# Performance work log

Measured on AMD Instinct MI355X. Metric: run time of the kernel, lower is better.

Reference implementation:

```python
import jax, jax.numpy as jnp
import numpy as np

N_NODES = 50000
N_EDGES = 800000
D_IN = 64
D_HID = 128  # out_channels * expansion(2)
EPS_MSG = 1e-7
EPS_SOFTMAX = 1e-16
EPS_BN = 1e-5
N_LAYERS = 4


def mish(x):
    return x * jnp.tanh(jax.nn.softplus(x))


def setup_inputs() -> dict:
    key = jax.random.key(0)
    ks = jax.random.split(key, 8)
    x = jax.random.normal(ks[0], (N_NODES, D_IN), dtype=jnp.float32)
    edge_index = jax.random.randint(ks[1], (2, N_EDGES), 0, N_NODES, dtype=jnp.int64)
    # Per-layer GENConv MLP params: Linear(64->128), BN(128), ReLU, Linear(128->64)
    s1 = 1.0 / np.sqrt(D_IN)
    s2 = 1.0 / np.sqrt(D_HID)
    W1 = jax.random.uniform(ks[2], (N_LAYERS, D_IN, D_HID), jnp.float32, -s1, s1)
    b1 = jax.random.uniform(ks[3], (N_LAYERS, D_HID), jnp.float32, -s1, s1)
    gamma = jnp.ones((N_LAYERS, D_HID), jnp.float32)
    beta = jnp.zeros((N_LAYERS, D_HID), jnp.float32)
    W2 = jax.random.uniform(ks[4], (N_LAYERS, D_HID, D_IN), jnp.float32, -s2, s2)
    b2 = jax.random.uniform(ks[5], (N_LAYERS, D_IN), jnp.float32, -s2, s2)
    return {"x": x, "edge_index": edge_index, "W1": W1, "b1": b1,
            "gamma": gamma, "beta": beta, "W2": W2, "b2": b2}


def gen_conv(x, src, dst, W1, b1, gamma, beta, W2, b2):
    n = x.shape[0]
    # message: relu(x_j) + eps  -> [E, D]
    msg = jax.nn.relu(x[src]) + EPS_MSG
    # softmax aggregation (t=1) per destination node, per feature channel
    m = jax.ops.segment_max(msg, dst, num_segments=n)
    e = jnp.exp(msg - m[dst])
    denom = jax.ops.segment_sum(e, dst, num_segments=n)[dst] + EPS_SOFTMAX
    alpha = e / denom
    agg = jax.ops.segment_sum(msg * alpha, dst, num_segments=n)
    # residual with destination features, then 2-layer MLP w/ BatchNorm (train mode)
    h = agg + x
    h = h @ W1 + b1
    mu = jnp.mean(h, axis=0)
    var = jnp.var(h, axis=0)  # biased, as torch BN uses for normalization
    h = (h - mu) * jax.lax.rsqrt(var + EPS_BN) * gamma + beta
    h = jax.nn.relu(h)
    return h @ W2 + b2


def reference(x, edge_index, W1, b1, gamma, beta, W2, b2):
    src, dst = edge_index[0], edge_index[1]
    h = x
    for i in range(N_LAYERS):
        h = gen_conv(h, src, dst, W1[i], b1[i], gamma[i], beta[i], W2[i], b2[i])
        if i < N_LAYERS - 1:
            h = mish(h)
    return h
```

## Files before the change

### kernel.cpp

```cpp
#include <hip/hip_runtime.h>
#include <math.h>

#define N_NODES 50000
#define N_EDGES 800000
#define D_IN 64
#define D_HID 128
#define SCAN_B 256
#define N_SB ((N_NODES + SCAN_B - 1) / SCAN_B)
#define NPB 256
#define NB ((N_NODES + NPB - 1) / NPB)
#define P1_BLOCKS 256
#define EPB (N_EDGES / P1_BLOCKS)

typedef unsigned short u16;
typedef unsigned int u32;
typedef __attribute__((ext_vector_type(8))) short short8;
typedef __attribute__((ext_vector_type(4))) float f32x4;

union U4S8 { uint4 u; short8 s; };

__device__ __forceinline__ float bf2f(u16 u) {
    u32 x = ((u32)u) << 16;
    float f; __builtin_memcpy(&f, &x, 4); return f;
}
__device__ __forceinline__ u16 f2bf(float f) {
    u32 x; __builtin_memcpy(&x, &f, 4);
    x += 0x7fffu + ((x >> 16) & 1u);
    return (u16)(x >> 16);
}
__device__ __forceinline__ u32 pk2(float a, float b) {
    return (u32)f2bf(a) | ((u32)f2bf(b) << 16);
}


__global__ void count_kernel(const int* __restrict__ dst, int* __restrict__ deg, int E) {
    int i = blockIdx.x * blockDim.x + threadIdx.x;
    if (i < E) atomicAdd(&deg[dst[i]], 1);
}

__global__ __launch_bounds__(SCAN_B) void scan_reduce_kernel(const int* __restrict__ deg,
                                                             int* __restrict__ bsum) {
    __shared__ int s[SCAN_B];
    int i = blockIdx.x * SCAN_B + threadIdx.x;
    int v = (i < N_NODES) ? deg[i] : 0;
    s[threadIdx.x] = v;
    __syncthreads();
    #pragma unroll
    for (int o = SCAN_B / 2; o > 0; o >>= 1) {
        if (threadIdx.x < o) s[threadIdx.x] += s[threadIdx.x + o];
        __syncthreads();
    }
    if (threadIdx.x == 0) bsum[blockIdx.x] = s[0];
}

__global__ __launch_bounds__(SCAN_B) void scan_sums_kernel(const int* __restrict__ bsum,
                                                           int* __restrict__ boff) {
    __shared__ int s[SCAN_B];
    int t = threadIdx.x;
    int v = (t < N_SB) ? bsum[t] : 0;
    s[t] = v;
    __syncthreads();
    #pragma unroll
    for (int o = 1; o < SCAN_B; o <<= 1) {
        int u = (t >= o) ? s[t - o] : 0;
        __syncthreads();
        s[t] += u;
        __syncthreads();
    }
    if (t < N_SB) boff[t] = s[t] - v;
}

__global__ __launch_bounds__(SCAN_B) void scan_write_kernel(const int* __restrict__ deg,
                                                            const int* __restrict__ boff,
                                                            int* __restrict__ off) {
    __shared__ int s[SCAN_B];
    int t = threadIdx.x;
    int i = blockIdx.x * SCAN_B + t;
    int v = (i < N_NODES) ? deg[i] : 0;
    s[t] = v;
    __syncthreads();
    #pragma unroll
    for (int o = 1; o < SCAN_B; o <<= 1) {
        int u = (t >= o) ? s[t - o] : 0;
        __syncthreads();
        s[t] += u;
        __syncthreads();
    }
    int incl = s[t] + boff[blockIdx.x];
    if (i < N_NODES) off[i] = incl - v;
    if (i == N_NODES - 1) off[N_NODES] = incl;
}

__global__ void bin_init_kernel(const int* __restrict__ off, int* __restrict__ gcur) {
    int b = threadIdx.x;
    if (b < NB) gcur[b] = off[min(b * NPB, N_NODES)];
}

__global__ __launch_bounds__(256) void bin_pass1_kernel(const int* __restrict__ src,
                                                        const int* __restrict__ dst,
                                                        int* __restrict__ gcur,
                                                        int2* __restrict__ ebuf) {
    __shared__ int hist[NB];
    __shared__ int base[NB];
    const int tid = threadIdx.x;
    const int e0 = blockIdx.x * EPB, e1 = e0 + EPB;
    for (int b = tid; b < NB; b += 256) hist[b] = 0;
    __syncthreads();
    for (int i = e0 + tid; i < e1; i += 256)
        atomicAdd(&hist[dst[i] >> 8], 1);
    __syncthreads();
    for (int b = tid; b < NB; b += 256) {
        base[b] = atomicAdd(&gcur[b], hist[b]);
        hist[b] = 0;
    }
    __syncthreads();
    for (int i = e0 + tid; i < e1; i += 256) {
        int d = dst[i];
        int b = d >> 8;
        int slot = base[b] + atomicAdd(&hist[b], 1);
        ebuf[slot] = make_int2(src[i], d);
    }
}

__global__ __launch_bounds__(256) void bin_pass2_kernel(const int* __restrict__ off,
                                                        const int2* __restrict__ ebuf,
                                                        int* __restrict__ esrc) {
    __shared__ int soff[NPB];
    __shared__ int cur[NPB];
    const int b = blockIdx.x;
    const int tid = threadIdx.x;
    const int n0 = b * NPB;
    soff[tid] = off[min(n0 + tid, N_NODES)];
    cur[tid] = 0;
    __syncthreads();
    const int e0 = soff[0];
    const int e1 = off[min(n0 + NPB, N_NODES)];
    for (int i = e0 + tid; i < e1; i += 256) {
        int2 p = ebuf[i];
        int dl = p.y - n0;
        int slot = soff[dl] + atomicAdd(&cur[dl], 1);
        esrc[slot] = p.x;
    }
}

__global__ __launch_bounds__(256) void xcvt_kernel(const float* __restrict__ x,
                                                   u16* __restrict__ xb) {
    int i = blockIdx.x * 256 + threadIdx.x;
    if (i < N_NODES * D_IN / 4) {
        float4 v = ((const float4*)x)[i];
        u32 lo = pk2(v.x, v.y), hi = pk2(v.z, v.w);
        ((uint2*)xb)[i] = make_uint2(lo, hi);
    }
}

__global__ __launch_bounds__(256) void wprep_kernel(const float* __restrict__ W1,
                                                    const float* __restrict__ W2,
                                                    u16* __restrict__ w1f,
                                                    u16* __restrict__ w2f) {
    const int b = blockIdx.x;
    const int L = b >> 1;
    if ((b & 1) == 0) {
        const float* W = W1 + (size_t)L * 64 * 128;
        u16* outp = w1f + (size_t)L * 8192;
        for (int idx = threadIdx.x; idx < 1024; idx += 256) {
            int ln = idx & 63, th = idx >> 6;
            int half = th & 1, t = th >> 1;
            int k0 = half * 32 + (ln >> 4) * 8;
            int n = t * 16 + (ln & 15);
            uint4 o;
            o.x = pk2(W[(k0 + 0) * 128 + n], W[(k0 + 1) * 128 + n]);
            o.y = pk2(W[(k0 + 2) * 128 + n], W[(k0 + 3) * 128 + n]);
            o.z = pk2(W[(k0 + 4) * 128 + n], W[(k0 + 5) * 128 + n]);
            o.w = pk2(W[(k0 + 6) * 128 + n], W[(k0 + 7) * 128 + n]);
            *(uint4*)&outp[(size_t)idx * 8] = o;
        }
    } else {
        const float* W = W2 + (size_t)L * 128 * 64;
        u16* outp = w2f + (size_t)L * 8192;
        for (int idx = threadIdx.x; idx < 1024; idx += 256) {
            int ln = idx & 63, th = idx >> 6;
            int ks = th & 3, t = th >> 2;
            int k0 = ks * 32 + (ln >> 4) * 8;
            int n = t * 16 + (ln & 15);
            uint4 o;
            o.x = pk2(W[(k0 + 0) * 64 + n], W[(k0 + 1) * 64 + n]);
            o.y = pk2(W[(k0 + 2) * 64 + n], W[(k0 + 3) * 64 + n]);
            o.z = pk2(W[(k0 + 4) * 64 + n], W[(k0 + 5) * 64 + n]);
            o.w = pk2(W[(k0 + 6) * 64 + n], W[(k0 + 7) * 64 + n]);
            *(uint4*)&outp[(size_t)idx * 8] = o;
        }
    }
}

__global__ __launch_bounds__(256) void agg_kernel(const u16* __restrict__ x,
                                                  const int* __restrict__ off,
                                                  const int* __restrict__ esrc,
                                                  u16* __restrict__ h) {
    const int node = blockIdx.x * 4 + (threadIdx.x >> 6);
    const int ln = threadIdx.x & 63;
    const int e = ln >> 3;
    const int cb = (ln & 7) * 8;
    if (node >= N_NODES) return;
    const int jb = off[node], je = off[node + 1];
    float s[8], t[8];
    #pragma unroll
    for (int k = 0; k < 8; k++) { s[k] = 0.f; t[k] = 0.f; }
    int j = jb;
    for (; j + 16 <= je; j += 16) {
        int i0 = esrc[j + e];
        int i1 = esrc[j + 8 + e];
        U4S8 r0, r1;
        r0.u = *(const uint4*)&x[(size_t)i0 * D_IN + cb];
        r1.u = *(const uint4*)&x[(size_t)i1 * D_IN + cb];
        #pragma unroll
        for (int k = 0; k < 8; k++) {
            float m = fmaxf(bf2f((u16)r0.s[k]), 0.f) + 1e-7f;
            float p = __expf(m);
            s[k] += p; t[k] = fmaf(m, p, t[k]);
        }
        #pragma unroll
        for (int k = 0; k < 8; k++) {
            float m = fmaxf(bf2f((u16)r1.s[k]), 0.f) + 1e-7f;
            float p = __expf(m);
            s[k] += p; t[k] = fmaf(m, p, t[k]);
        }
    }
    int rem = je - j;
    if (rem > 0) {
        bool act = e < rem;
        int idx = esrc[j + (act ? e : rem - 1)];
        U4S8 r;
        r.u = *(const uint4*)&x[(size_t)idx * D_IN + cb];
        if (act) {
            #pragma unroll
            for (int k = 0; k < 8; k++) {
                float m = fmaxf(bf2f((u16)r.s[k]), 0.f) + 1e-7f;
                float p = __expf(m);
                s[k] += p; t[k] = fmaf(m, p, t[k]);
            }
        }
        if (rem > 8) {
            bool act2 = (e + 8) < rem;
            int idx2 = esrc[j + 8 + (act2 ? e : rem - 9)];
            U4S8 r2;
            r2.u = *(const uint4*)&x[(size_t)idx2 * D_IN + cb];
            if (act2) {
                #pragma unroll
                for (int k = 0; k < 8; k++) {
                    float m = fmaxf(bf2f((u16)r2.s[k]), 0.f) + 1e-7f;
                    float p = __expf(m);
                    s[k] += p; t[k] = fmaf(m, p, t[k]);
                }
            }
        }
    }
    #pragma unroll
    for (int k = 0; k < 8; k++) {
        s[k] += __shfl_xor(s[k], 8);
        s[k] += __shfl_xor(s[k], 16);
        s[k] += __shfl_xor(s[k], 32);
        t[k] += __shfl_xor(t[k], 8);
        t[k] += __shfl_xor(t[k], 16);
        t[k] += __shfl_xor(t[k], 32);
    }
    if (e == 0) {
        U4S8 xr;
        xr.u = *(const uint4*)&x[(size_t)node * D_IN + cb];
        u32 w[4];
        #pragma unroll
        for (int k2 = 0; k2 < 4; k2++) {
            float v0 = t[2 * k2]     / (s[2 * k2]     + 1e-16f) + bf2f((u16)xr.s[2 * k2]);
            float v1 = t[2 * k2 + 1] / (s[2 * k2 + 1] + 1e-16f) + bf2f((u16)xr.s[2 * k2 + 1]);
            w[k2] = pk2(v0, v1);
        }
        *(uint4*)&h[(size_t)node * D_IN + cb] = make_uint4(w[0], w[1], w[2], w[3]);
    }
}

#define SC1 136
__global__ __launch_bounds__(256) void gemm1_kernel(const u16* __restrict__ A,
                                                    const u16* __restrict__ Wf,
                                                    const float* __restrict__ bias,
                                                    u16* __restrict__ Bout,
                                                    float* __restrict__ S,
                                                    float* __restrict__ Q) {
    __shared__ u16 sC[64 * SC1];
    const int tid = threadIdx.x;
    const int wave = tid >> 6, ln = tid & 63;
    const int lm = ln & 15, quad = ln >> 4;
    const int row0g = blockIdx.x * 64;
    const int row0 = row0g + wave * 16;
    const int rA = min(row0 + lm, N_NODES - 1);

    U4S8 a0, a1;
    a0.u = *(const uint4*)&A[(size_t)rA * 64 + quad * 8];
    a1.u = *(const uint4*)&A[(size_t)rA * 64 + 32 + quad * 8];

    f32x4 acc[8];
    #pragma unroll
    for (int t = 0; t < 8; t++) {
        float b = bias[t * 16 + lm];
        acc[t] = (f32x4){b, b, b, b};
    }
    #pragma unroll
    for (int t = 0; t < 8; t++) {
        U4S8 b0, b1;
        b0.u = *(const uint4*)&Wf[(size_t)((t * 2 + 0) * 64 + ln) * 8];
        b1.u = *(const uint4*)&Wf[(size_t)((t * 2 + 1) * 64 + ln) * 8];
        acc[t] = __builtin_amdgcn_mfma_f32_16x16x32_bf16(a0.s, b0.s, acc[t], 0, 0, 0);
        acc[t] = __builtin_amdgcn_mfma_f32_16x16x32_bf16(a1.s, b1.s, acc[t], 0, 0, 0);
    }
    const int lr0 = wave * 16 + quad * 4;
    #pragma unroll
    for (int t = 0; t < 8; t++) {
        #pragma unroll
        for (int rg = 0; rg < 4; rg++)
            sC[(lr0 + rg) * SC1 + t * 16 + lm] = f2bf(acc[t][rg]);
    }
    __syncthreads();
    const int c8 = (tid & 15) * 8;
    #pragma unroll
    for (int i = 0; i < 4; i++) {
        int lr = (tid >> 4) + i * 16;
        int r = row0g + lr;
        if (r < N_NODES)
            *(uint4*)&Bout[(size_t)r * 128 + c8] = *(const uint4*)&sC[lr * SC1 + c8];
    }
    const int rlim = min(64, N_NODES - row0g);
    if (tid < 128) {
        float s = 0.f;
        #pragma unroll 8
        for (int r = 0; r < rlim; r++) s += bf2f(sC[r * SC1 + tid]);
        atomicAdd(&S[tid], s);
    } else {
        int c = tid - 128;
        float q = 0.f;
        #pragma unroll 8
        for (int r = 0; r < rlim; r++) { float v = bf2f(sC[r * SC1 + c]); q += v * v; }
        atomicAdd(&Q[c], q);
    }
}

__device__ __forceinline__ float mish_f(float v) {
    if (v > 30.f) return v;
    float u = __expf(v);
    float t = (u + 1.f) * (u + 1.f);
    return v * (t - 1.f) / (t + 1.f);
}

#define SC2B 72
#define SC2F 68
__global__ __launch_bounds__(256) void gemm2_kernel(const u16* __restrict__ H,
                                                    const float* __restrict__ S,
                                                    const float* __restrict__ Q,
                                                    const float* __restrict__ gamma,
                                                    const float* __restrict__ beta,
                                                    const u16* __restrict__ Wf,
                                                    const float* __restrict__ bias,
                                                    float* __restrict__ outf,
                                                    u16* __restrict__ outb,
                                                    int dobf16) {
    __shared__ float sss[256];
    __shared__ __align__(16) char sCraw[64 * SC2F * 4];
    u16* sCb = (u16*)sCraw;
    float* sCf = (float*)sCraw;
    const int tid = threadIdx.x;
    if (tid < 128) {
        float mean = S[tid] * (1.f / N_NODES);
        float var = fmaxf(Q[tid] * (1.f / N_NODES) - mean * mean, 0.f);
        float sc = gamma[tid] * rsqrtf(var + 1e-5f);
        sss[tid] = sc;
        sss[128 + tid] = beta[tid] - mean * sc;
    }
    __syncthreads();
    const int wave = tid >> 6, ln = tid & 63;
    const int lm = ln & 15, quad = ln >> 4;
    const int row0g = blockIdx.x * 64;
    const int row0 = row0g + wave * 16;
    const int rA = min(row0 + lm, N_NODES - 1);

    f32x4 acc[4];
    #pragma unroll
    for (int t = 0; t < 4; t++) {
        float b = bias[t * 16 + lm];
        acc[t] = (f32x4){b, b, b, b};
    }
    #pragma unroll
    for (int ks = 0; ks < 4; ks++) {
        const int k0 = ks * 32 + quad * 8;
        U4S8 h8;
        h8.u = *(const uint4*)&H[(size_t)rA * 128 + k0];
        U4S8 a;
        #pragma unroll
        for (int j2 = 0; j2 < 4; j2++) {
            int k = k0 + 2 * j2;
            float v0 = fmaxf(fmaf(bf2f((u16)h8.s[2 * j2]),     sss[k],     sss[128 + k]),     0.f);
            float v1 = fmaxf(fmaf(bf2f((u16)h8.s[2 * j2 + 1]), sss[k + 1], sss[128 + k + 1]), 0.f);
            ((u32*)&a.u)[j2] = pk2(v0, v1);
        }
        #pragma unroll
        for (int t = 0; t < 4; t++) {
            U4S8 b;
            b.u = *(const uint4*)&Wf[(size_t)((t * 4 + ks) * 64 + ln) * 8];
            acc[t] = __builtin_amdgcn_mfma_f32_16x16x32_bf16(a.s, b.s, acc[t], 0, 0, 0);
        }
    }
    const int lr0 = wave * 16 + quad * 4;
    if (dobf16) {
        #pragma unroll
        for (int t = 0; t < 4; t++) {
            #pragma unroll
            for (int rg = 0; rg < 4; rg++)
                sCb[(lr0 + rg) * SC2B + t * 16 + lm] = f2bf(mish_f(acc[t][rg]));
        }
        __syncthreads();
        const int c8 = (tid & 7) * 8;
        #pragma unroll
        for (int i = 0; i < 2; i++) {
            int lr = (tid >> 3) + i * 32;
            int r = row0g + lr;
            if (r < N_NODES)
                *(uint4*)&outb[(size_t)r * 64 + c8] = *(const uint4*)&sCb[lr * SC2B + c8];
        }
    } else {
        #pragma unroll
        for (int t = 0; t < 4; t++) {
            #pragma unroll
            for (int rg = 0; rg < 4; rg++)
                sCf[(lr0 + rg) * SC2F + t * 16 + lm] = acc[t][rg];
        }
        __syncthreads();
        const int c8 = (tid & 7) * 8;
        #pragma unroll
        for (int i = 0; i < 2; i++) {
            int lr = (tid >> 3) + i * 32;
            int r = row0g + lr;
            if (r < N_NODES) {
                *(float4*)&outf[(size_t)r * 64 + c8]     = *(const float4*)&sCf[lr * SC2F + c8];
                *(float4*)&outf[(size_t)r * 64 + c8 + 4] = *(const float4*)&sCf[lr * SC2F + c8 + 4];
            }
        }
    }
}


extern "C" void kernel_launch(void* const* d_in, const int* in_sizes, int n_in,
                              void* d_out, int out_size, void* d_ws, size_t ws_size,
                              hipStream_t stream) {
    const float* x     = (const float*)d_in[0];
    const int*   ei    = (const int*)d_in[1];
    const float* W1    = (const float*)d_in[2];
    const float* b1    = (const float*)d_in[3];
    const float* gamma = (const float*)d_in[4];
    const float* beta  = (const float*)d_in[5];
    const float* W2    = (const float*)d_in[6];
    const float* b2    = (const float*)d_in[7];
    float* out = (float*)d_out;

    const int* src = ei;
    const int* dst = ei + N_EDGES;

    char* base = (char*)d_ws;
    size_t o = 0;
    auto take = [&](size_t bytes) -> char* {
        char* p = base + o;
        o = (o + bytes + 255) & ~(size_t)255;
        return p;
    };
    int* deg     = (int*)take((size_t)N_NODES * 4);
    int* off     = (int*)take((size_t)(N_NODES + 1) * 4);
    int* esrc    = (int*)take((size_t)N_EDGES * 4);
    int2* ebuf   = (int2*)take((size_t)N_EDGES * 8);
    int* bsum    = (int*)take((size_t)N_SB * 4);
    int* boff    = (int*)take((size_t)N_SB * 4);
    int* gcur    = (int*)take((size_t)NB * 4);
    float* bn    = (float*)take(1024 * 4);
    u16* w1f     = (u16*)take((size_t)4 * 8192 * 2);
    u16* w2f     = (u16*)take((size_t)4 * 8192 * 2);
    u16* xbuf    = (u16*)take((size_t)N_NODES * D_IN * 2);
    u16* hbuf    = (u16*)take((size_t)N_NODES * D_IN * 2);
    u16* h1buf   = (u16*)take((size_t)N_NODES * D_HID * 2);

    hipMemsetAsync(deg, 0, (size_t)N_NODES * 4, stream);
    hipMemsetAsync(bn, 0, 1024 * 4, stream);
    count_kernel<<<(N_EDGES + 255) / 256, 256, 0, stream>>>(dst, deg, N_EDGES);
    scan_reduce_kernel<<<N_SB, SCAN_B, 0, stream>>>(deg, bsum);
    scan_sums_kernel<<<1, SCAN_B, 0, stream>>>(bsum, boff);
    scan_write_kernel<<<N_SB, SCAN_B, 0, stream>>>(deg, boff, off);
    bin_init_kernel<<<1, 256, 0, stream>>>(off, gcur);
    bin_pass1_kernel<<<P1_BLOCKS, 256, 0, stream>>>(src, dst, gcur, ebuf);
    bin_pass2_kernel<<<NB, 256, 0, stream>>>(off, ebuf, esrc);
    xcvt_kernel<<<(N_NODES * D_IN / 4 + 255) / 256, 256, 0, stream>>>(x, xbuf);
    wprep_kernel<<<8, 256, 0, stream>>>(W1, W2, w1f, w2f);

    const int NBLK = (N_NODES + 63) / 64;
    const int ABLK = (N_NODES + 3) / 4;
    for (int L = 0; L < 4; L++) {
        float* Sb = bn + L * 256;
        float* Qb = Sb + 128;
        agg_kernel<<<ABLK, 256, 0, stream>>>(xbuf, off, esrc, hbuf);
        gemm1_kernel<<<NBLK, 256, 0, stream>>>(
            hbuf, w1f + (size_t)L * 8192, b1 + (size_t)L * D_HID, h1buf,
            Sb, Qb);
        gemm2_kernel<<<NBLK, 256, 0, stream>>>(
            h1buf, Sb, Qb, gamma + (size_t)L * D_HID, beta + (size_t)L * D_HID,
            w2f + (size_t)L * 8192, b2 + (size_t)L * D_IN,
            out, xbuf, (L < 3) ? 1 : 0);
    }
}
```

Measured before the change: 438.3 us.

## Split node features into two channel halves and aggregate each half separately

Node features are stored as two 32-channel bf16 arrays, and the aggregation runs twice, once per half, so each gather pass has a smaller working set that fits better in cache. Each aggregation kernel now covers 16 edges per iteration with 4 lanes per row, and uses nontemporal loads and stores for edge indices and outputs. Separately, gemm1 computes the BatchNorm sum and sum-of-squares from fp32 MFMA accumulators through shuffles instead of rescanning bf16 values in shared memory. The cost is twice the edge-index reads and an extra kernel launch per layer.

```diff
diff --git a/kernel.cpp b/kernel.cpp
--- a/kernel.cpp
+++ b/kernel.cpp
@@ -16,6 +16,7 @@
 typedef unsigned int u32;
 typedef __attribute__((ext_vector_type(8))) short short8;
 typedef __attribute__((ext_vector_type(4))) float f32x4;
+typedef __attribute__((ext_vector_type(4))) u32 u32x4;
 
 union U4S8 { uint4 u; short8 s; };
 
@@ -144,12 +145,19 @@
 }
 
 __global__ __launch_bounds__(256) void xcvt_kernel(const float* __restrict__ x,
-                                                   u16* __restrict__ xb) {
+                                                   u16* __restrict__ xlo,
+                                                   u16* __restrict__ xhi) {
     int i = blockIdx.x * 256 + threadIdx.x;
     if (i < N_NODES * D_IN / 4) {
         float4 v = ((const float4*)x)[i];
+        int node = i >> 4;
+        int c4 = (i & 15) * 4;
         u32 lo = pk2(v.x, v.y), hi = pk2(v.z, v.w);
-        ((uint2*)xb)[i] = make_uint2(lo, hi);
+        uint2 o = make_uint2(lo, hi);
+        if (c4 < 32)
+            *(uint2*)&xlo[(size_t)node * 32 + c4] = o;
+        else
+            *(uint2*)&xhi[(size_t)node * 32 + (c4 - 32)] = o;
     }
 }
 
@@ -192,45 +200,39 @@
     }
 }
 
-__global__ __launch_bounds__(256) void agg_kernel(const u16* __restrict__ x,
-                                                  const int* __restrict__ off,
-                                                  const int* __restrict__ esrc,
-                                                  u16* __restrict__ h) {
+__global__ __launch_bounds__(256) void agg32_kernel(const u16* __restrict__ xh,
+                                                    const int* __restrict__ off,
+                                                    const int* __restrict__ esrc,
+                                                    u16* __restrict__ h,
+                                                    int chbase) {
     const int node = blockIdx.x * 4 + (threadIdx.x >> 6);
     const int ln = threadIdx.x & 63;
-    const int e = ln >> 3;
-    const int cb = (ln & 7) * 8;
-    if (node >= N_NODES) return;
+    const int e = ln >> 2;
+    const int cb = (ln & 3) * 8;
     const int jb = off[node], je = off[node + 1];
+    U4S8 xr;
+    xr.u = *(const uint4*)&xh[(size_t)node * 32 + cb];
     float s[8], t[8];
     #pragma unroll
     for (int k = 0; k < 8; k++) { s[k] = 0.f; t[k] = 0.f; }
     int j = jb;
     for (; j + 16 <= je; j += 16) {
-        int i0 = esrc[j + e];
-        int i1 = esrc[j + 8 + e];
-        U4S8 r0, r1;
-        r0.u = *(const uint4*)&x[(size_t)i0 * D_IN + cb];
-        r1.u = *(const uint4*)&x[(size_t)i1 * D_IN + cb];
+        int i0 = __builtin_nontemporal_load(&esrc[j + e]);
+        U4S8 r0;
+        r0.u = *(const uint4*)&xh[(size_t)i0 * 32 + cb];
         #pragma unroll
         for (int k = 0; k < 8; k++) {
             float m = fmaxf(bf2f((u16)r0.s[k]), 0.f) + 1e-7f;
             float p = __expf(m);
             s[k] += p; t[k] = fmaf(m, p, t[k]);
         }
-        #pragma unroll
-        for (int k = 0; k < 8; k++) {
-            float m = fmaxf(bf2f((u16)r1.s[k]), 0.f) + 1e-7f;
-            float p = __expf(m);
-            s[k] += p; t[k] = fmaf(m, p, t[k]);
-        }
     }
     int rem = je - j;
     if (rem > 0) {
         bool act = e < rem;
-        int idx = esrc[j + (act ? e : rem - 1)];
+        int idx = __builtin_nontemporal_load(&esrc[j + (act ? e : 0)]);
         U4S8 r;
-        r.u = *(const uint4*)&x[(size_t)idx * D_IN + cb];
+        r.u = *(const uint4*)&xh[(size_t)idx * 32 + cb];
         if (act) {
             #pragma unroll
             for (int k = 0; k < 8; k++) {
@@ -239,41 +241,23 @@
                 s[k] += p; t[k] = fmaf(m, p, t[k]);
             }
         }
-        if (rem > 8) {
-            bool act2 = (e + 8) < rem;
-            int idx2 = esrc[j + 8 + (act2 ? e : rem - 9)];
-            U4S8 r2;
-            r2.u = *(const uint4*)&x[(size_t)idx2 * D_IN + cb];
-            if (act2) {
-                #pragma unroll
-                for (int k = 0; k < 8; k++) {
-                    float m = fmaxf(bf2f((u16)r2.s[k]), 0.f) + 1e-7f;
-                    float p = __expf(m);
-                    s[k] += p; t[k] = fmaf(m, p, t[k]);
-                }
-            }
-        }
     }
     #pragma unroll
     for (int k = 0; k < 8; k++) {
-        s[k] += __shfl_xor(s[k], 8);
-        s[k] += __shfl_xor(s[k], 16);
-        s[k] += __shfl_xor(s[k], 32);
-        t[k] += __shfl_xor(t[k], 8);
-        t[k] += __shfl_xor(t[k], 16);
-        t[k] += __shfl_xor(t[k], 32);
+        s[k] += __shfl_xor(s[k], 4);  s[k] += __shfl_xor(s[k], 8);
+        s[k] += __shfl_xor(s[k], 16); s[k] += __shfl_xor(s[k], 32);
+        t[k] += __shfl_xor(t[k], 4);  t[k] += __shfl_xor(t[k], 8);
+        t[k] += __shfl_xor(t[k], 16); t[k] += __shfl_xor(t[k], 32);
     }
     if (e == 0) {
-        U4S8 xr;
-        xr.u = *(const uint4*)&x[(size_t)node * D_IN + cb];
-        u32 w[4];
+        u32x4 w;
         #pragma unroll
         for (int k2 = 0; k2 < 4; k2++) {
             float v0 = t[2 * k2]     / (s[2 * k2]     + 1e-16f) + bf2f((u16)xr.s[2 * k2]);
             float v1 = t[2 * k2 + 1] / (s[2 * k2 + 1] + 1e-16f) + bf2f((u16)xr.s[2 * k2 + 1]);
             w[k2] = pk2(v0, v1);
         }
-        *(uint4*)&h[(size_t)node * D_IN + cb] = make_uint4(w[0], w[1], w[2], w[3]);
+        __builtin_nontemporal_store(w, (u32x4*)&h[(size_t)node * 64 + chbase + cb]);
     }
 }
 
@@ -285,6 +269,7 @@
                                                     float* __restrict__ S,
                                                     float* __restrict__ Q) {
     __shared__ u16 sC[64 * SC1];
+    __shared__ float sRed[2][4][128];
     const int tid = threadIdx.x;
     const int wave = tid >> 6, ln = tid & 63;
     const int lm = ln & 15, quad = ln >> 4;
@@ -310,6 +295,24 @@
         acc[t] = __builtin_amdgcn_mfma_f32_16x16x32_bf16(a0.s, b0.s, acc[t], 0, 0, 0);
         acc[t] = __builtin_amdgcn_mfma_f32_16x16x32_bf16(a1.s, b1.s, acc[t], 0, 0, 0);
     }
+    const int rbase = row0 + quad * 4;
+    #pragma unroll
+    for (int t = 0; t < 8; t++) {
+        float ss = 0.f, qq = 0.f;
+        #pragma unroll
+        for (int rg = 0; rg < 4; rg++) {
+            if (rbase + rg < N_NODES) {
+                float v = acc[t][rg];
+                ss += v; qq = fmaf(v, v, qq);
+            }
+        }
+        ss += __shfl_xor(ss, 16); ss += __shfl_xor(ss, 32);
+        qq += __shfl_xor(qq, 16); qq += __shfl_xor(qq, 32);
+        if (quad == 0) {
+            sRed[0][wave][t * 16 + lm] = ss;
+            sRed[1][wave][t * 16 + lm] = qq;
+        }
+    }
     const int lr0 = wave * 16 + quad * 4;
     #pragma unroll
     for (int t = 0; t < 8; t++) {
@@ -326,18 +329,13 @@
         if (r < N_NODES)
             *(uint4*)&Bout[(size_t)r * 128 + c8] = *(const uint4*)&sC[lr * SC1 + c8];
     }
-    const int rlim = min(64, N_NODES - row0g);
     if (tid < 128) {
-        float s = 0.f;
-        #pragma unroll 8
-        for (int r = 0; r < rlim; r++) s += bf2f(sC[r * SC1 + tid]);
-        atomicAdd(&S[tid], s);
+        float v = sRed[0][0][tid] + sRed[0][1][tid] + sRed[0][2][tid] + sRed[0][3][tid];
+        atomicAdd(&S[tid], v);
     } else {
         int c = tid - 128;
-        float q = 0.f;
-        #pragma unroll 8
-        for (int r = 0; r < rlim; r++) { float v = bf2f(sC[r * SC1 + c]); q += v * v; }
-        atomicAdd(&Q[c], q);
+        float v = sRed[1][0][c] + sRed[1][1][c] + sRed[1][2][c] + sRed[1][3][c];
+        atomicAdd(&Q[c], v);
     }
 }
 
@@ -358,7 +356,8 @@
                                                     const u16* __restrict__ Wf,
                                                     const float* __restrict__ bias,
                                                     float* __restrict__ outf,
-                                                    u16* __restrict__ outb,
+                                                    u16* __restrict__ xlo,
+                                                    u16* __restrict__ xhi,
                                                     int dobf16) {
     __shared__ float sss[256];
     __shared__ __align__(16) char sCraw[64 * SC2F * 4];
@@ -419,8 +418,13 @@
         for (int i = 0; i < 2; i++) {
             int lr = (tid >> 3) + i * 32;
             int r = row0g + lr;
-            if (r < N_NODES)
-                *(uint4*)&outb[(size_t)r * 64 + c8] = *(const uint4*)&sCb[lr * SC2B + c8];
+            if (r < N_NODES) {
+                uint4 val = *(const uint4*)&sCb[lr * SC2B + c8];
+                if (c8 < 32)
+                    *(uint4*)&xlo[(size_t)r * 32 + c8] = val;
+                else
+                    *(uint4*)&xhi[(size_t)r * 32 + (c8 - 32)] = val;
+            }
         }
     } else {
         #pragma unroll
@@ -477,7 +481,8 @@
     float* bn    = (float*)take(1024 * 4);
     u16* w1f     = (u16*)take((size_t)4 * 8192 * 2);
     u16* w2f     = (u16*)take((size_t)4 * 8192 * 2);
-    u16* xbuf    = (u16*)take((size_t)N_NODES * D_IN * 2);
+    u16* xlo     = (u16*)take((size_t)N_NODES * 32 * 2);
+    u16* xhi     = (u16*)take((size_t)N_NODES * 32 * 2);
     u16* hbuf    = (u16*)take((size_t)N_NODES * D_IN * 2);
     u16* h1buf   = (u16*)take((size_t)N_NODES * D_HID * 2);
 
@@ -490,7 +495,7 @@
     bin_init_kernel<<<1, 256, 0, stream>>>(off, gcur);
     bin_pass1_kernel<<<P1_BLOCKS, 256, 0, stream>>>(src, dst, gcur, ebuf);
     bin_pass2_kernel<<<NB, 256, 0, stream>>>(off, ebuf, esrc);
-    xcvt_kernel<<<(N_NODES * D_IN / 4 + 255) / 256, 256, 0, stream>>>(x, xbuf);
+    xcvt_kernel<<<(N_NODES * D_IN / 4 + 255) / 256, 256, 0, stream>>>(x, xlo, xhi);
     wprep_kernel<<<8, 256, 0, stream>>>(W1, W2, w1f, w2f);
 
     const int NBLK = (N_NODES + 63) / 64;
@@ -498,13 +503,14 @@
     for (int L = 0; L < 4; L++) {
         float* Sb = bn + L * 256;
         float* Qb = Sb + 128;
-        agg_kernel<<<ABLK, 256, 0, stream>>>(xbuf, off, esrc, hbuf);
+        agg32_kernel<<<ABLK, 256, 0, stream>>>(xlo, off, esrc, hbuf, 0);
+        agg32_kernel<<<ABLK, 256, 0, stream>>>(xhi, off, esrc, hbuf, 32);
         gemm1_kernel<<<NBLK, 256, 0, stream>>>(
             hbuf, w1f + (size_t)L * 8192, b1 + (size_t)L * D_HID, h1buf,
             Sb, Qb);
         gemm2_kernel<<<NBLK, 256, 0, stream>>>(
             h1buf, Sb, Qb, gamma + (size_t)L * D_HID, beta + (size_t)L * D_HID,
             w2f + (size_t)L * 8192, b2 + (size_t)L * D_IN,
-            out, xbuf, (L < 3) ? 1 : 0);
-    }
-}
+            out, xlo, xhi, (L < 3) ? 1 : 0);
+    }
+}
```

Result: slower. 598.6 us (+36.6%).

## Precompute ReLU'd bf16 features and compute BN stats from accumulators

Applied to the files above, without the earlier changes.

Producer kernels now write a second bf16 buffer holding relu(x), so the gather loop in aggregation skips the max and epsilon add per element. The constant epsilon is added after normalisation, which is exact because the softmax weights sum to about one. The exp is also taken without the epsilon, which changes rounding slightly. Gemm1 now reduces BN sum and sum-of-squares from fp32 MFMA accumulators with wave shuffles and a small shared buffer, replacing the serial 64-row loop over bf16 shared memory. The cost is an extra 6.4 MB buffer and an extra store per layer.

```diff
diff --git a/kernel.cpp b/kernel.cpp
--- a/kernel.cpp
+++ b/kernel.cpp
@@ -31,6 +31,12 @@
 __device__ __forceinline__ u32 pk2(float a, float b) {
     return (u32)f2bf(a) | ((u32)f2bf(b) << 16);
 }
+__device__ __forceinline__ u32 relu2(u32 w) {
+    u32 b = (w >> 15) & 0x00010001u;
+    u32 m01 = b ^ 0x00010001u;
+    u32 M = (m01 << 16) - m01;
+    return w & M;
+}
 
 
 __global__ void count_kernel(const int* __restrict__ dst, int* __restrict__ deg, int E) {
@@ -144,12 +150,14 @@
 }
 
 __global__ __launch_bounds__(256) void xcvt_kernel(const float* __restrict__ x,
-                                                   u16* __restrict__ xb) {
+                                                   u16* __restrict__ xb,
+                                                   u16* __restrict__ rb) {
     int i = blockIdx.x * 256 + threadIdx.x;
     if (i < N_NODES * D_IN / 4) {
         float4 v = ((const float4*)x)[i];
         u32 lo = pk2(v.x, v.y), hi = pk2(v.z, v.w);
         ((uint2*)xb)[i] = make_uint2(lo, hi);
+        ((uint2*)rb)[i] = make_uint2(relu2(lo), relu2(hi));
     }
 }
 
@@ -192,7 +200,8 @@
     }
 }
 
-__global__ __launch_bounds__(256) void agg_kernel(const u16* __restrict__ x,
+__global__ __launch_bounds__(256) void agg_kernel(const u16* __restrict__ xb,
+                                                  const u16* __restrict__ rb,
                                                   const int* __restrict__ off,
                                                   const int* __restrict__ esrc,
                                                   u16* __restrict__ h) {
@@ -202,6 +211,8 @@
     const int cb = (ln & 7) * 8;
     if (node >= N_NODES) return;
     const int jb = off[node], je = off[node + 1];
+    U4S8 xr;
+    xr.u = *(const uint4*)&xb[(size_t)node * D_IN + cb];
     float s[8], t[8];
     #pragma unroll
     for (int k = 0; k < 8; k++) { s[k] = 0.f; t[k] = 0.f; }
@@ -210,17 +221,17 @@
         int i0 = esrc[j + e];
         int i1 = esrc[j + 8 + e];
         U4S8 r0, r1;
-        r0.u = *(const uint4*)&x[(size_t)i0 * D_IN + cb];
-        r1.u = *(const uint4*)&x[(size_t)i1 * D_IN + cb];
+        r0.u = *(const uint4*)&rb[(size_t)i0 * D_IN + cb];
+        r1.u = *(const uint4*)&rb[(size_t)i1 * D_IN + cb];
         #pragma unroll
         for (int k = 0; k < 8; k++) {
-            float m = fmaxf(bf2f((u16)r0.s[k]), 0.f) + 1e-7f;
+            float m = bf2f((u16)r0.s[k]);
             float p = __expf(m);
             s[k] += p; t[k] = fmaf(m, p, t[k]);
         }
         #pragma unroll
         for (int k = 0; k < 8; k++) {
-            float m = fmaxf(bf2f((u16)r1.s[k]), 0.f) + 1e-7f;
+            float m = bf2f((u16)r1.s[k]);
             float p = __expf(m);
             s[k] += p; t[k] = fmaf(m, p, t[k]);
         }
@@ -230,11 +241,11 @@
         bool act = e < rem;
         int idx = esrc[j + (act ? e : rem - 1)];
         U4S8 r;
-        r.u = *(const uint4*)&x[(size_t)idx * D_IN + cb];
+        r.u = *(const uint4*)&rb[(size_t)idx * D_IN + cb];
         if (act) {
             #pragma unroll
             for (int k = 0; k < 8; k++) {
-                float m = fmaxf(bf2f((u16)r.s[k]), 0.f) + 1e-7f;
+                float m = bf2f((u16)r.s[k]);
                 float p = __expf(m);
                 s[k] += p; t[k] = fmaf(m, p, t[k]);
             }
@@ -243,11 +254,11 @@
             bool act2 = (e + 8) < rem;
             int idx2 = esrc[j + 8 + (act2 ? e : rem - 9)];
             U4S8 r2;
-            r2.u = *(const uint4*)&x[(size_t)idx2 * D_IN + cb];
+            r2.u = *(const uint4*)&rb[(size_t)idx2 * D_IN + cb];
             if (act2) {
                 #pragma unroll
                 for (int k = 0; k < 8; k++) {
-                    float m = fmaxf(bf2f((u16)r2.s[k]), 0.f) + 1e-7f;
+                    float m = bf2f((u16)r2.s[k]);
                     float p = __expf(m);
                     s[k] += p; t[k] = fmaf(m, p, t[k]);
                 }
@@ -264,13 +275,11 @@
         t[k] += __shfl_xor(t[k], 32);
     }
     if (e == 0) {
-        U4S8 xr;
-        xr.u = *(const uint4*)&x[(size_t)node * D_IN + cb];
         u32 w[4];
         #pragma unroll
         for (int k2 = 0; k2 < 4; k2++) {
-            float v0 = t[2 * k2]     / (s[2 * k2]     + 1e-16f) + bf2f((u16)xr.s[2 * k2]);
-            float v1 = t[2 * k2 + 1] / (s[2 * k2 + 1] + 1e-16f) + bf2f((u16)xr.s[2 * k2 + 1]);
+            float v0 = t[2 * k2]     / (s[2 * k2]     + 1e-16f) + 1e-7f + bf2f((u16)xr.s[2 * k2]);
+            float v1 = t[2 * k2 + 1] / (s[2 * k2 + 1] + 1e-16f) + 1e-7f + bf2f((u16)xr.s[2 * k2 + 1]);
             w[k2] = pk2(v0, v1);
         }
         *(uint4*)&h[(size_t)node * D_IN + cb] = make_uint4(w[0], w[1], w[2], w[3]);
@@ -285,6 +294,7 @@
                                                     float* __restrict__ S,
                                                     float* __restrict__ Q) {
     __shared__ u16 sC[64 * SC1];
+    __shared__ float sRed[2][4][128];
     const int tid = threadIdx.x;
     const int wave = tid >> 6, ln = tid & 63;
     const int lm = ln & 15, quad = ln >> 4;
@@ -310,6 +320,24 @@
         acc[t] = __builtin_amdgcn_mfma_f32_16x16x32_bf16(a0.s, b0.s, acc[t], 0, 0, 0);
         acc[t] = __builtin_amdgcn_mfma_f32_16x16x32_bf16(a1.s, b1.s, acc[t], 0, 0, 0);
     }
+    const int rbase = row0 + quad * 4;
+    #pragma unroll
+    for (int t = 0; t < 8; t++) {
+        float ss = 0.f, qq = 0.f;
+        #pragma unroll
+        for (int rg = 0; rg < 4; rg++) {
+            if (rbase + rg < N_NODES) {
+                float v = acc[t][rg];
+                ss += v; qq = fmaf(v, v, qq);
+            }
+        }
+        ss += __shfl_xor(ss, 16); ss += __shfl_xor(ss, 32);
+        qq += __shfl_xor(qq, 16); qq += __shfl_xor(qq, 32);
+        if (quad == 0) {
+            sRed[0][wave][t * 16 + lm] = ss;
+            sRed[1][wave][t * 16 + lm] = qq;
+        }
+    }
     const int lr0 = wave * 16 + quad * 4;
     #pragma unroll
     for (int t = 0; t < 8; t++) {
@@ -326,18 +354,13 @@
         if (r < N_NODES)
             *(uint4*)&Bout[(size_t)r * 128 + c8] = *(const uint4*)&sC[lr * SC1 + c8];
     }
-    const int rlim = min(64, N_NODES - row0g);
     if (tid < 128) {
-        float s = 0.f;
-        #pragma unroll 8
-        for (int r = 0; r < rlim; r++) s += bf2f(sC[r * SC1 + tid]);
-        atomicAdd(&S[tid], s);
+        float v = sRed[0][0][tid] + sRed[0][1][tid] + sRed[0][2][tid] + sRed[0][3][tid];
+        atomicAdd(&S[tid], v);
     } else {
         int c = tid - 128;
-        float q = 0.f;
-        #pragma unroll 8
-        for (int r = 0; r < rlim; r++) { float v = bf2f(sC[r * SC1 + c]); q += v * v; }
-        atomicAdd(&Q[c], q);
+        float v = sRed[1][0][c] + sRed[1][1][c] + sRed[1][2][c] + sRed[1][3][c];
+        atomicAdd(&Q[c], v);
     }
 }
 
@@ -358,7 +381,8 @@
                                                     const u16* __restrict__ Wf,
                                                     const float* __restrict__ bias,
                                                     float* __restrict__ outf,
-                                                    u16* __restrict__ outb,
+                                                    u16* __restrict__ xb,
+                                                    u16* __restrict__ rb,
                                                     int dobf16) {
     __shared__ float sss[256];
     __shared__ __align__(16) char sCraw[64 * SC2F * 4];
@@ -419,8 +443,14 @@
         for (int i = 0; i < 2; i++) {
             int lr = (tid >> 3) + i * 32;
             int r = row0g + lr;
-            if (r < N_NODES)
-                *(uint4*)&outb[(size_t)r * 64 + c8] = *(const uint4*)&sCb[lr * SC2B + c8];
+            if (r < N_NODES) {
+                uint4 val = *(const uint4*)&sCb[lr * SC2B + c8];
+                *(uint4*)&xb[(size_t)r * 64 + c8] = val;
+                uint4 rv;
+                rv.x = relu2(val.x); rv.y = relu2(val.y);
+                rv.z = relu2(val.z); rv.w = relu2(val.w);
+                *(uint4*)&rb[(size_t)r * 64 + c8] = rv;
+            }
         }
     } else {
         #pragma unroll
@@ -478,6 +508,7 @@
     u16* w1f     = (u16*)take((size_t)4 * 8192 * 2);
     u16* w2f     = (u16*)take((size_t)4 * 8192 * 2);
     u16* xbuf    = (u16*)take((size_t)N_NODES * D_IN * 2);
+    u16* rbuf    = (u16*)take((size_t)N_NODES * D_IN * 2);
     u16* hbuf    = (u16*)take((size_t)N_NODES * D_IN * 2);
     u16* h1buf   = (u16*)take((size_t)N_NODES * D_HID * 2);
 
@@ -490,7 +521,7 @@
     bin_init_kernel<<<1, 256, 0, stream>>>(off, gcur);
     bin_pass1_kernel<<<P1_BLOCKS, 256, 0, stream>>>(src, dst, gcur, ebuf);
     bin_pass2_kernel<<<NB, 256, 0, stream>>>(off, ebuf, esrc);
-    xcvt_kernel<<<(N_NODES * D_IN / 4 + 255) / 256, 256, 0, stream>>>(x, xbuf);
+    xcvt_kernel<<<(N_NODES * D_IN / 4 + 255) / 256, 256, 0, stream>>>(x, xbuf, rbuf);
     wprep_kernel<<<8, 256, 0, stream>>>(W1, W2, w1f, w2f);
 
     const int NBLK = (N_NODES + 63) / 64;
@@ -498,13 +529,13 @@
     for (int L = 0; L < 4; L++) {
         float* Sb = bn + L * 256;
         float* Qb = Sb + 128;
-        agg_kernel<<<ABLK, 256, 0, stream>>>(xbuf, off, esrc, hbuf);
+        agg_kernel<<<ABLK, 256, 0, stream>>>(xbuf, rbuf, off, esrc, hbuf);
         gemm1_kernel<<<NBLK, 256, 0, stream>>>(
             hbuf, w1f + (size_t)L * 8192, b1 + (size_t)L * D_HID, h1buf,
             Sb, Qb);
         gemm2_kernel<<<NBLK, 256, 0, stream>>>(
             h1buf, Sb, Qb, gamma + (size_t)L * D_HID, beta + (size_t)L * D_HID,
             w2f + (size_t)L * 8192, b2 + (size_t)L * D_IN,
-            out, xbuf, (L < 3) ? 1 : 0);
-    }
-}
+            out, xbuf, rbuf, (L < 3) ? 1 : 0);
+    }
+}
```

New measurement: 433.9 us. About the same (-1.0%).
